# Performance work log

Measured on AMD Instinct MI355X. Metric: run time of the kernel, lower is better.

## Reference

```python
import jax, jax.numpy as jnp
import numpy as np

B, E, T = 2, 512, 2048
H = 8
LOCAL_SIZE = 128
NEG_INF = -1e9


def setup_inputs() -> dict:
    key = jax.random.key(0)
    ks = jax.random.split(key, 5)
    return {
        "x": jax.random.normal(ks[0], (B, E, T), dtype=jnp.float32),
        "in_proj_w": jax.random.normal(ks[1], (3 * E, E), dtype=jnp.float32) * (E ** -0.5),
        "in_proj_b": jax.random.normal(ks[2], (3 * E,), dtype=jnp.float32) * 0.02,
        "out_w": jax.random.normal(ks[3], (E, E), dtype=jnp.float32) * (E ** -0.5),
        "out_b": jax.random.normal(ks[4], (E,), dtype=jnp.float32) * 0.02,
    }


def _local_mask(t, local_size, dtype):
    # allowed iff |i - j| <= local_size // 2 (sliding local window)
    i = jnp.arange(t)[:, None]
    j = jnp.arange(t)[None, :]
    allowed = jnp.abs(i - j) <= (local_size // 2)
    return jnp.where(allowed, jnp.zeros((), dtype), jnp.full((), NEG_INF, dtype))


def reference(x, in_proj_w, in_proj_b, out_w, out_b):
    dh = E // H
    scale = 1.0 / jnp.sqrt(jnp.asarray(dh, x.dtype))
    xt = jnp.transpose(x, (0, 2, 1))               # [B, T, E]
    qkv = xt @ in_proj_w.T + in_proj_b             # [B, T, 3E]
    q, k, v = jnp.split(qkv, 3, axis=-1)
    q = q.reshape(B, T, H, dh)
    k = k.reshape(B, T, H, dh)
    v = v.reshape(B, T, H, dh)
    scores = jnp.einsum("bqhd,bkhd->bhqk", q, k) * scale  # [B, H, T, T]
    scores = scores + _local_mask(T, LOCAL_SIZE, scores.dtype)
    attn = jax.nn.softmax(scores, axis=-1)
    ctx = jnp.einsum("bhqk,bkhd->bqhd", attn, v).reshape(B, T, E)
    attn_out = ctx @ out_w.T + out_b               # [B, T, E]
    attn_out = jnp.transpose(attn_out, (0, 2, 1))  # [B, E, T]
    return jax.nn.relu(attn_out * x)
```

## Files before the change

### kernel.cpp

```cpp
#include <hip/hip_runtime.h>
#include <stdint.h>


#define DEVI __device__ __forceinline__

typedef __attribute__((ext_vector_type(8))) short bf16x8;
typedef __attribute__((ext_vector_type(4))) float f32x4;

DEVI unsigned short f2bf(float f) {
  unsigned u = __float_as_uint(f);
  u += 0x7fffu + ((u >> 16) & 1u);
  return (unsigned short)(u >> 16);
}
DEVI float bf2f(unsigned short h) { return __uint_as_float(((unsigned)h) << 16); }

#define GLL16(gp, lp)                                                          \
  __builtin_amdgcn_global_load_lds(                                            \
      (const __attribute__((address_space(1))) void*)(gp),                     \
      (__attribute__((address_space(3))) void*)(lp), 16, 0, 0)

#define MFMA(a, b, c) __builtin_amdgcn_mfma_f32_16x16x32_bf16((a), (b), (c), 0, 0, 0)

__global__ __launch_bounds__(256) void k_prep(
    const float* __restrict__ x, const float* __restrict__ w_in,
    const float* __restrict__ w_out, unsigned short* __restrict__ xh,
    unsigned short* __restrict__ wih, unsigned short* __restrict__ woh) {
  const int tid = threadIdx.x;
  if (blockIdx.y == 16) {
    int cb = (blockIdx.z << 6) | blockIdx.x;
    const float* src;
    unsigned short* dst;
    int base;
    if (cb < 96) {
      src = w_in; dst = wih; base = cb * 8192;
    } else {
      src = w_out; dst = woh; base = (cb - 96) * 8192;
    }
#pragma unroll
    for (int k = 0; k < 8; k++) {
      int idx = base + (k * 256 + tid) * 4;
      float4 v = *(const float4*)&src[idx];
      ushort4 o;
      o.x = f2bf(v.x); o.y = f2bf(v.y); o.z = f2bf(v.z); o.w = f2bf(v.w);
      *(ushort4*)&dst[idx] = o;
    }
    return;
  }
  __shared__ float tile[32][33];
  const int b = blockIdx.z, e0 = blockIdx.y * 32, t0 = blockIdx.x * 32;
  const int j = tid & 31, i = tid >> 5;
#pragma unroll
  for (int rr = 0; rr < 4; rr++) {
    int e = e0 + i + rr * 8;
    tile[i + rr * 8][j] = x[((size_t)b * 512 + e) * 2048 + t0 + j];
  }
  __syncthreads();
#pragma unroll
  for (int rr = 0; rr < 4; rr++) {
    int t = t0 + i + rr * 8;
    float v = tile[j][i + rr * 8];
    size_t o = ((size_t)b * 2048 + t) * 512 + e0 + j;
    xh[o] = f2bf(v);
  }
}

__global__ __launch_bounds__(256) void k_gemm_qkv(
    const unsigned short* __restrict__ Ahg, const unsigned short* __restrict__ Bhg,
    const float* __restrict__ bias, unsigned short* __restrict__ Qs,
    unsigned short* __restrict__ Kks, unsigned short* __restrict__ Vvs) {
  const int KD = 512;
  __shared__ __align__(16) unsigned short Ah_s[128 * 32];
  __shared__ __align__(16) unsigned short Bh_s[128 * 32];
  const int tid = threadIdx.x, lane = tid & 63, w = tid >> 6;
  const int bid = blockIdx.x;
  const int xcd = bid & 7, j5 = bid >> 3;
  const int m0 = (xcd * 4 + j5 / 12) * 128, n0 = (j5 % 12) * 128;
  const int wm = (w >> 1) * 64, wn = (w & 1) * 64;

  f32x4 acc[4][4];
#pragma unroll
  for (int i = 0; i < 4; i++)
#pragma unroll
    for (int j = 0; j < 4; j++) acc[i][j] = (f32x4){0.f, 0.f, 0.f, 0.f};

  const int srw = lane >> 2, sc = (lane & 3) * 8;
  const size_t b0 = (size_t)(n0 + w * 32 + srw) * KD + sc;
  const size_t b1 = b0 + (size_t)16 * KD;
  unsigned short* lB0 = &Bh_s[(w * 32) * 32];
  unsigned short* lB1 = &Bh_s[(w * 32 + 16) * 32];
  const size_t a0 = (size_t)(m0 + w * 32 + srw) * KD + sc;
  const size_t a1 = a0 + (size_t)16 * KD;
  unsigned short* lAh0 = &Ah_s[(w * 32) * 32];
  unsigned short* lAh1 = &Ah_s[(w * 32 + 16) * 32];

  const int fm = lane & 15, fq = (lane >> 4) * 8;

  for (int k0 = 0; k0 < KD; k0 += 32) {
    __syncthreads();
    GLL16(Ahg + a0 + k0, lAh0);
    GLL16(Ahg + a1 + k0, lAh1);
    GLL16(Bhg + b0 + k0, lB0);
    GLL16(Bhg + b1 + k0, lB1);
    __builtin_amdgcn_s_waitcnt(0);
    __syncthreads();

    bf16x8 ah[4], bh[4];
#pragma unroll
    for (int i = 0; i < 4; i++) {
      ah[i] = *(const bf16x8*)&Ah_s[(wm + i * 16 + fm) * 32 + fq];
      bh[i] = *(const bf16x8*)&Bh_s[(wn + i * 16 + fm) * 32 + fq];
    }
#pragma unroll
    for (int i = 0; i < 4; i++)
#pragma unroll
      for (int j = 0; j < 4; j++)
        acc[i][j] = MFMA(ah[i], bh[j], acc[i][j]);
  }

  const int quad = lane >> 4;
#pragma unroll
  for (int i = 0; i < 4; i++)
#pragma unroll
    for (int j = 0; j < 4; j++) {
      int gn = n0 + wn + j * 16 + fm;
      float bv = bias[gn];
      int sec = gn >> 9, cc = gn & 511;
      int h = cc >> 6, d = cc & 63;
      unsigned short* dst = sec == 0 ? Qs : (sec == 1 ? Kks : Vvs);
      float mul = sec == 0 ? 0.125f : 1.0f;
#pragma unroll
      for (int r = 0; r < 4; r++) {
        int gm = m0 + wm + i * 16 + quad * 4 + r;
        int bb = gm >> 11, t = gm & 2047;
        float v = (acc[i][j][r] + bv) * mul;
        dst[(((size_t)(bb * 8 + h)) * 2048 + t) * 64 + d] = f2bf(v);
      }
    }
}

__global__ __launch_bounds__(256) void k_gemm_out(
    const unsigned short* __restrict__ Ahg, const unsigned short* __restrict__ Alg,
    const unsigned short* __restrict__ Bhg, const float* __restrict__ bias,
    const float* __restrict__ x, float* __restrict__ out) {
  const int KD = 512;
  __shared__ __align__(16) union {
    struct {
      unsigned short Ah[64 * 32];
      unsigned short Al[64 * 32];
      unsigned short Bh[128 * 32];
    } st;
    float tile[64][129];
  } u;
  const int tid = threadIdx.x, lane = tid & 63, w = tid >> 6;
  const int bid = blockIdx.x;
  const int xcd = bid & 7, j5 = bid >> 3;
  const int m0 = (xcd * 8 + (j5 >> 2)) * 64, n0 = (j5 & 3) * 128;
  const int wm = (w >> 1) * 32, wn = (w & 1) * 64;

  f32x4 acc[2][4];
#pragma unroll
  for (int i = 0; i < 2; i++)
#pragma unroll
    for (int j = 0; j < 4; j++) acc[i][j] = (f32x4){0.f, 0.f, 0.f, 0.f};

  const int srw = lane >> 2, sc = (lane & 3) * 8;
  const size_t b0 = (size_t)(n0 + w * 32 + srw) * KD + sc;
  const size_t b1 = b0 + (size_t)16 * KD;
  const size_t a0 = (size_t)(m0 + w * 16 + srw) * KD + sc;
  unsigned short* lB0 = &u.st.Bh[(w * 32) * 32];
  unsigned short* lB1 = &u.st.Bh[(w * 32 + 16) * 32];
  unsigned short* lAh0 = &u.st.Ah[(w * 16) * 32];
  unsigned short* lAl0 = &u.st.Al[(w * 16) * 32];

  const int fm = lane & 15, fq = (lane >> 4) * 8;

  for (int k0 = 0; k0 < KD; k0 += 32) {
    __syncthreads();
    GLL16(Ahg + a0 + k0, lAh0);
    GLL16(Alg + a0 + k0, lAl0);
    GLL16(Bhg + b0 + k0, lB0);
    GLL16(Bhg + b1 + k0, lB1);
    __builtin_amdgcn_s_waitcnt(0);
    __syncthreads();

    bf16x8 ah[2], al[2], bh[4];
#pragma unroll
    for (int i = 0; i < 2; i++) {
      ah[i] = *(const bf16x8*)&u.st.Ah[(wm + i * 16 + fm) * 32 + fq];
      al[i] = *(const bf16x8*)&u.st.Al[(wm + i * 16 + fm) * 32 + fq];
    }
#pragma unroll
    for (int j = 0; j < 4; j++)
      bh[j] = *(const bf16x8*)&u.st.Bh[(wn + j * 16 + fm) * 32 + fq];
#pragma unroll
    for (int i = 0; i < 2; i++)
#pragma unroll
      for (int j = 0; j < 4; j++) {
        acc[i][j] = MFMA(ah[i], bh[j], acc[i][j]);
        acc[i][j] = MFMA(al[i], bh[j], acc[i][j]);
      }
  }

  __syncthreads();
  const int quad = lane >> 4;
#pragma unroll
  for (int i = 0; i < 2; i++)
#pragma unroll
    for (int j = 0; j < 4; j++) {
      int ln = wn + j * 16 + fm;
      float bv = bias[n0 + ln];
#pragma unroll
      for (int r = 0; r < 4; r++) {
        int lm = wm + i * 16 + quad * 4 + r;
        u.tile[lm][ln] = acc[i][j][r] + bv;
      }
    }
  __syncthreads();

  const int bb = m0 >> 11, t0 = m0 & 2047;
  const int tt = tid & 63, e0w = tid >> 6;
#pragma unroll
  for (int k = 0; k < 32; k++) {
    int ee = e0w + k * 4;
    size_t o = ((size_t)bb * 512 + n0 + ee) * 2048 + t0 + tt;
    float v = u.tile[tt][ee] * x[o];
    out[o] = fmaxf(v, 0.f);
  }
}

#define KSTR 88
#define VSTR 216
__global__ __launch_bounds__(256) void k_attention(
    const unsigned short* __restrict__ Qs, const unsigned short* __restrict__ Kks,
    const unsigned short* __restrict__ Vvs, unsigned short* __restrict__ ctx_hi,
    unsigned short* __restrict__ ctx_lo) {
  __shared__ __align__(16) unsigned short KP_s[192 * KSTR];
  __shared__ __align__(16) unsigned short Vt_s[64 * VSTR];
  __shared__ float redm[4 * 64];
  __shared__ float reds[4 * 64];

  const int tid = threadIdx.x, lane = tid & 63, w = tid >> 6;
  const int q0 = blockIdx.x * 64;
  const int bh = blockIdx.y;
  const int j0 = q0 - 64;
  const size_t base = (size_t)bh * 2048 * 64;

  for (int idx = tid; idx < 192 * 8; idx += 256) {
    int r = idx >> 3, c = idx & 7;
    int j = j0 + r;
    j = j < 0 ? 0 : (j > 2047 ? 2047 : j);
    uint4 v = *(const uint4*)&Kks[base + (size_t)j * 64 + c * 8];
    *(uint4*)&KP_s[r * KSTR + c * 8] = v;
  }
  for (int idx = tid; idx < 192 * 8; idx += 256) {
    int r = idx >> 3, c8 = (idx & 7) * 8;
    int j = j0 + r;
    uint4 v;
    if (j >= 0 && j < 2048)
      v = *(const uint4*)&Vvs[base + (size_t)j * 64 + c8];
    else
      v = (uint4){0u, 0u, 0u, 0u};
    const unsigned short* e = (const unsigned short*)&v;
#pragma unroll
    for (int uu = 0; uu < 8; uu++) Vt_s[(c8 + uu) * VSTR + r] = e[uu];
  }

  const int fm = lane & 15, quad = lane >> 4;
  bf16x8 aq[4][2];
#pragma unroll
  for (int mt = 0; mt < 4; mt++)
#pragma unroll
    for (int ks = 0; ks < 2; ks++)
      aq[mt][ks] = *(const bf16x8*)&Qs[base + (size_t)(q0 + mt * 16 + fm) * 64 +
                                       ks * 32 + quad * 8];
  __syncthreads();

  const int n0s = w * 48;
  f32x4 s_acc[4][3];
#pragma unroll
  for (int mt = 0; mt < 4; mt++)
#pragma unroll
    for (int nt = 0; nt < 3; nt++) s_acc[mt][nt] = (f32x4){0.f, 0.f, 0.f, 0.f};
#pragma unroll
  for (int nt = 0; nt < 3; nt++)
#pragma unroll
    for (int ks = 0; ks < 2; ks++) {
      bf16x8 bk =
          *(const bf16x8*)&KP_s[(n0s + nt * 16 + fm) * KSTR + ks * 32 + quad * 8];
#pragma unroll
      for (int mt = 0; mt < 4; mt++) s_acc[mt][nt] = MFMA(aq[mt][ks], bk, s_acc[mt][nt]);
    }

  float rm[4][4];
#pragma unroll
  for (int mt = 0; mt < 4; mt++)
#pragma unroll
    for (int r = 0; r < 4; r++) rm[mt][r] = -1e30f;
#pragma unroll
  for (int mt = 0; mt < 4; mt++)
#pragma unroll
    for (int nt = 0; nt < 3; nt++) {
      int jj = n0s + nt * 16 + fm;
      int jg = j0 + jj;
#pragma unroll
      for (int r = 0; r < 4; r++) {
        int ii = mt * 16 + quad * 4 + r;
        bool ok = (jj >= ii) && (jj <= ii + 128) && (jg >= 0) && (jg < 2048);
        float sv = ok ? s_acc[mt][nt][r] : -1e30f;
        s_acc[mt][nt][r] = sv;
        rm[mt][r] = fmaxf(rm[mt][r], sv);
      }
    }
#pragma unroll
  for (int off = 1; off < 16; off <<= 1)
#pragma unroll
    for (int mt = 0; mt < 4; mt++)
#pragma unroll
      for (int r = 0; r < 4; r++)
        rm[mt][r] = fmaxf(rm[mt][r], __shfl_xor(rm[mt][r], off));
  if (fm == 0)
#pragma unroll
    for (int mt = 0; mt < 4; mt++)
#pragma unroll
      for (int r = 0; r < 4; r++)
        redm[w * 64 + mt * 16 + quad * 4 + r] = rm[mt][r];
  __syncthreads();
  float fmx[4][4];
#pragma unroll
  for (int mt = 0; mt < 4; mt++)
#pragma unroll
    for (int r = 0; r < 4; r++) {
      int row = mt * 16 + quad * 4 + r;
      fmx[mt][r] = fmaxf(fmaxf(redm[row], redm[64 + row]),
                         fmaxf(redm[128 + row], redm[192 + row]));
    }
  float rs[4][4];
#pragma unroll
  for (int mt = 0; mt < 4; mt++)
#pragma unroll
    for (int r = 0; r < 4; r++) rs[mt][r] = 0.f;
#pragma unroll
  for (int mt = 0; mt < 4; mt++)
#pragma unroll
    for (int nt = 0; nt < 3; nt++)
#pragma unroll
      for (int r = 0; r < 4; r++) {
        float e = __expf(s_acc[mt][nt][r] - fmx[mt][r]);
        s_acc[mt][nt][r] = e;
        rs[mt][r] += e;
      }
#pragma unroll
  for (int off = 1; off < 16; off <<= 1)
#pragma unroll
    for (int mt = 0; mt < 4; mt++)
#pragma unroll
      for (int r = 0; r < 4; r++) rs[mt][r] += __shfl_xor(rs[mt][r], off);
  if (fm == 0)
#pragma unroll
    for (int mt = 0; mt < 4; mt++)
#pragma unroll
      for (int r = 0; r < 4; r++)
        reds[w * 64 + mt * 16 + quad * 4 + r] = rs[mt][r];
  __syncthreads();
  float inv[4][4];
#pragma unroll
  for (int mt = 0; mt < 4; mt++)
#pragma unroll
    for (int r = 0; r < 4; r++) {
      int row = mt * 16 + quad * 4 + r;
      inv[mt][r] =
          1.0f / (reds[row] + reds[64 + row] + reds[128 + row] + reds[192 + row]);
    }
#pragma unroll
  for (int mt = 0; mt < 4; mt++)
#pragma unroll
    for (int nt = 0; nt < 3; nt++) {
      int col = n0s + nt * 16 + fm;
#pragma unroll
      for (int r = 0; r < 4; r++) {
        int row = mt * 16 + quad * 4 + r;
        KP_s[row * VSTR + col] = f2bf(s_acc[mt][nt][r] * inv[mt][r]);
      }
    }
  __syncthreads();

  const int n0v = w * 16;
  f32x4 o_acc[4];
#pragma unroll
  for (int mt = 0; mt < 4; mt++) o_acc[mt] = (f32x4){0.f, 0.f, 0.f, 0.f};
#pragma unroll
  for (int ks = 0; ks < 6; ks++) {
    bf16x8 bv = *(const bf16x8*)&Vt_s[(n0v + fm) * VSTR + ks * 32 + quad * 8];
#pragma unroll
    for (int mt = 0; mt < 4; mt++) {
      bf16x8 ap = *(const bf16x8*)&KP_s[(mt * 16 + fm) * VSTR + ks * 32 + quad * 8];
      o_acc[mt] = MFMA(ap, bv, o_acc[mt]);
    }
  }
  const int bb = bh >> 3, h = bh & 7;
#pragma unroll
  for (int mt = 0; mt < 4; mt++)
#pragma unroll
    for (int r = 0; r < 4; r++) {
      int t = q0 + mt * 16 + quad * 4 + r;
      int c = h * 64 + n0v + fm;
      float v = o_acc[mt][r];
      unsigned short hv = f2bf(v);
      size_t o = ((size_t)(bb * 2048 + t)) * 512 + c;
      ctx_hi[o] = hv;
      ctx_lo[o] = f2bf(v - bf2f(hv));
    }
}

extern "C" void kernel_launch(void* const* d_in, const int* in_sizes, int n_in,
                              void* d_out, int out_size, void* d_ws, size_t ws_size,
                              hipStream_t stream) {
  const float* x = (const float*)d_in[0];
  const float* w_in = (const float*)d_in[1];
  const float* b_in = (const float*)d_in[2];
  const float* w_out = (const float*)d_in[3];
  const float* b_out = (const float*)d_in[4];
  float* out = (float*)d_out;

  uint8_t* ws = (uint8_t*)d_ws;
  unsigned short* xT_hi = (unsigned short*)(ws + 0);
  unsigned short* wih   = (unsigned short*)(ws + 8388608);
  unsigned short* woh   = (unsigned short*)(ws + 9961472);
  unsigned short* Qs    = (unsigned short*)(ws + 12582912);
  unsigned short* Kk    = (unsigned short*)(ws + 16777216);
  unsigned short* Vv    = (unsigned short*)(ws + 20971520);
  unsigned short* ctxh  = (unsigned short*)(ws + 25165824);
  unsigned short* ctxl  = (unsigned short*)(ws + 29360128);

  k_prep<<<dim3(64, 17, 2), 256, 0, stream>>>(x, w_in, w_out, xT_hi, wih, woh);
  k_gemm_qkv<<<384, 256, 0, stream>>>(xT_hi, wih, b_in, Qs, Kk, Vv);
  k_attention<<<dim3(32, 16), 256, 0, stream>>>(Qs, Kk, Vv, ctxh, ctxl);
  k_gemm_out<<<256, 256, 0, stream>>>(ctxh, ctxl, woh, b_out, x, out);
}
```

Measured before the change: 117.4 us.

## Drop bf16 hi/lo split for context and store V pre-transposed

The attention output is written as a single bf16 tensor instead of a hi/lo pair. This halves the A-operand loads and MFMAs in the output projection and removes the second context write. The QKV GEMM now writes V transposed (d-major), so attention loads V rows into LDS with 16-byte stores instead of a scalar transpose scatter. The cost is lower accuracy in the context activations feeding the output GEMM.

```diff
diff --git a/kernel.cpp b/kernel.cpp
--- a/kernel.cpp
+++ b/kernel.cpp
@@ -67,7 +67,7 @@
 __global__ __launch_bounds__(256) void k_gemm_qkv(
     const unsigned short* __restrict__ Ahg, const unsigned short* __restrict__ Bhg,
     const float* __restrict__ bias, unsigned short* __restrict__ Qs,
-    unsigned short* __restrict__ Kks, unsigned short* __restrict__ Vvs) {
+    unsigned short* __restrict__ Kks, unsigned short* __restrict__ VvT) {
   const int KD = 512;
   __shared__ __align__(16) unsigned short Ah_s[128 * 32];
   __shared__ __align__(16) unsigned short Bh_s[128 * 32];
@@ -126,27 +126,35 @@
       float bv = bias[gn];
       int sec = gn >> 9, cc = gn & 511;
       int h = cc >> 6, d = cc & 63;
-      unsigned short* dst = sec == 0 ? Qs : (sec == 1 ? Kks : Vvs);
-      float mul = sec == 0 ? 0.125f : 1.0f;
-#pragma unroll
-      for (int r = 0; r < 4; r++) {
-        int gm = m0 + wm + i * 16 + quad * 4 + r;
-        int bb = gm >> 11, t = gm & 2047;
-        float v = (acc[i][j][r] + bv) * mul;
-        dst[(((size_t)(bb * 8 + h)) * 2048 + t) * 64 + d] = f2bf(v);
+      int gm0 = m0 + wm + i * 16 + quad * 4;
+      int bb = gm0 >> 11, t = gm0 & 2047;
+      if (sec == 2) {
+        ushort4 pk;
+        pk.x = f2bf(acc[i][j][0] + bv);
+        pk.y = f2bf(acc[i][j][1] + bv);
+        pk.z = f2bf(acc[i][j][2] + bv);
+        pk.w = f2bf(acc[i][j][3] + bv);
+        *(ushort4*)&VvT[(((size_t)(bb * 8 + h)) * 64 + d) * 2048 + t] = pk;
+      } else {
+        unsigned short* dst = sec == 0 ? Qs : Kks;
+        float mul = sec == 0 ? 0.125f : 1.0f;
+#pragma unroll
+        for (int r = 0; r < 4; r++) {
+          float v = (acc[i][j][r] + bv) * mul;
+          dst[(((size_t)(bb * 8 + h)) * 2048 + t + r) * 64 + d] = f2bf(v);
+        }
       }
     }
 }
 
 __global__ __launch_bounds__(256) void k_gemm_out(
-    const unsigned short* __restrict__ Ahg, const unsigned short* __restrict__ Alg,
-    const unsigned short* __restrict__ Bhg, const float* __restrict__ bias,
-    const float* __restrict__ x, float* __restrict__ out) {
+    const unsigned short* __restrict__ Ahg, const unsigned short* __restrict__ Bhg,
+    const float* __restrict__ bias, const float* __restrict__ x,
+    float* __restrict__ out) {
   const int KD = 512;
   __shared__ __align__(16) union {
     struct {
       unsigned short Ah[64 * 32];
-      unsigned short Al[64 * 32];
       unsigned short Bh[128 * 32];
     } st;
     float tile[64][129];
@@ -170,35 +178,29 @@
   unsigned short* lB0 = &u.st.Bh[(w * 32) * 32];
   unsigned short* lB1 = &u.st.Bh[(w * 32 + 16) * 32];
   unsigned short* lAh0 = &u.st.Ah[(w * 16) * 32];
-  unsigned short* lAl0 = &u.st.Al[(w * 16) * 32];
 
   const int fm = lane & 15, fq = (lane >> 4) * 8;
 
   for (int k0 = 0; k0 < KD; k0 += 32) {
     __syncthreads();
     GLL16(Ahg + a0 + k0, lAh0);
-    GLL16(Alg + a0 + k0, lAl0);
     GLL16(Bhg + b0 + k0, lB0);
     GLL16(Bhg + b1 + k0, lB1);
     __builtin_amdgcn_s_waitcnt(0);
     __syncthreads();
 
-    bf16x8 ah[2], al[2], bh[4];
-#pragma unroll
-    for (int i = 0; i < 2; i++) {
+    bf16x8 ah[2], bh[4];
+#pragma unroll
+    for (int i = 0; i < 2; i++)
       ah[i] = *(const bf16x8*)&u.st.Ah[(wm + i * 16 + fm) * 32 + fq];
-      al[i] = *(const bf16x8*)&u.st.Al[(wm + i * 16 + fm) * 32 + fq];
-    }
 #pragma unroll
     for (int j = 0; j < 4; j++)
       bh[j] = *(const bf16x8*)&u.st.Bh[(wn + j * 16 + fm) * 32 + fq];
 #pragma unroll
     for (int i = 0; i < 2; i++)
 #pragma unroll
-      for (int j = 0; j < 4; j++) {
+      for (int j = 0; j < 4; j++)
         acc[i][j] = MFMA(ah[i], bh[j], acc[i][j]);
-        acc[i][j] = MFMA(al[i], bh[j], acc[i][j]);
-      }
   }
 
   __syncthreads();
@@ -232,8 +234,7 @@
 #define VSTR 216
 __global__ __launch_bounds__(256) void k_attention(
     const unsigned short* __restrict__ Qs, const unsigned short* __restrict__ Kks,
-    const unsigned short* __restrict__ Vvs, unsigned short* __restrict__ ctx_hi,
-    unsigned short* __restrict__ ctx_lo) {
+    const unsigned short* __restrict__ VvT, unsigned short* __restrict__ ctx_hi) {
   __shared__ __align__(16) unsigned short KP_s[192 * KSTR];
   __shared__ __align__(16) unsigned short Vt_s[64 * VSTR];
   __shared__ float redm[4 * 64];
@@ -252,17 +253,15 @@
     uint4 v = *(const uint4*)&Kks[base + (size_t)j * 64 + c * 8];
     *(uint4*)&KP_s[r * KSTR + c * 8] = v;
   }
-  for (int idx = tid; idx < 192 * 8; idx += 256) {
-    int r = idx >> 3, c8 = (idx & 7) * 8;
-    int j = j0 + r;
+  for (int idx = tid; idx < 64 * 24; idx += 256) {
+    int d = idx / 24, c8 = (idx % 24) * 8;
+    int j = j0 + c8;
     uint4 v;
     if (j >= 0 && j < 2048)
-      v = *(const uint4*)&Vvs[base + (size_t)j * 64 + c8];
+      v = *(const uint4*)&VvT[base + (size_t)d * 2048 + j];
     else
       v = (uint4){0u, 0u, 0u, 0u};
-    const unsigned short* e = (const unsigned short*)&v;
-#pragma unroll
-    for (int uu = 0; uu < 8; uu++) Vt_s[(c8 + uu) * VSTR + r] = e[uu];
+    *(uint4*)&Vt_s[d * VSTR + c8] = v;
   }
 
   const int fm = lane & 15, quad = lane >> 4;
@@ -404,11 +403,7 @@
     for (int r = 0; r < 4; r++) {
       int t = q0 + mt * 16 + quad * 4 + r;
       int c = h * 64 + n0v + fm;
-      float v = o_acc[mt][r];
-      unsigned short hv = f2bf(v);
-      size_t o = ((size_t)(bb * 2048 + t)) * 512 + c;
-      ctx_hi[o] = hv;
-      ctx_lo[o] = f2bf(v - bf2f(hv));
+      ctx_hi[((size_t)(bb * 2048 + t)) * 512 + c] = f2bf(o_acc[mt][r]);
     }
 }
 
@@ -428,12 +423,11 @@
   unsigned short* woh   = (unsigned short*)(ws + 9961472);
   unsigned short* Qs    = (unsigned short*)(ws + 12582912);
   unsigned short* Kk    = (unsigned short*)(ws + 16777216);
-  unsigned short* Vv    = (unsigned short*)(ws + 20971520);
+  unsigned short* VvT   = (unsigned short*)(ws + 20971520);
   unsigned short* ctxh  = (unsigned short*)(ws + 25165824);
-  unsigned short* ctxl  = (unsigned short*)(ws + 29360128);
 
   k_prep<<<dim3(64, 17, 2), 256, 0, stream>>>(x, w_in, w_out, xT_hi, wih, woh);
-  k_gemm_qkv<<<384, 256, 0, stream>>>(xT_hi, wih, b_in, Qs, Kk, Vv);
-  k_attention<<<dim3(32, 16), 256, 0, stream>>>(Qs, Kk, Vv, ctxh, ctxl);
-  k_gemm_out<<<256, 256, 0, stream>>>(ctxh, ctxl, woh, b_out, x, out);
-}
+  k_gemm_qkv<<<384, 256, 0, stream>>>(xT_hi, wih, b_in, Qs, Kk, VvT);
+  k_attention<<<dim3(32, 16), 256, 0, stream>>>(Qs, Kk, VvT, ctxh);
+  k_gemm_out<<<256, 256, 0, stream>>>(ctxh, woh, b_out, x, out);
+}
```

Result: no change. 115.3 us (median of 2 runs) (-1.8%).
